# Optimization experiments

Hardware: AMD Instinct MI355X
Metric: run time of the kernel (lower is better)

Reference implementation:

```python
import jax, jax.numpy as jnp
import numpy as np

D_MODEL = 1024
STATE = 16
EXPAND = 2
D_INNER = D_MODEL * EXPAND
KCONV = 4


def setup_inputs() -> dict:
    key = jax.random.key(0)
    ks = jax.random.split(key, 8)
    s = 0.02  # small init scale for stability
    return {
        "x": jax.random.normal(ks[0], (2, 2048, D_MODEL), jnp.float32),
        "W_in": jax.random.normal(ks[1], (2 * D_INNER, D_MODEL), jnp.float32) * s,
        "conv_w": jax.random.normal(ks[2], (D_INNER, 1, KCONV), jnp.float32) * s,
        "conv_b": jnp.zeros((D_INNER,), jnp.float32),
        # A negative so exp(delta*A) <= 1 (stable recurrence, as in real Mamba init)
        "A": -jnp.abs(jax.random.normal(ks[3], (D_INNER, STATE), jnp.float32)),
        "W_x": jax.random.normal(ks[4], (2 * STATE + 1, D_INNER), jnp.float32) * s,
        "W_dt": jax.random.normal(ks[5], (D_INNER, 1), jnp.float32) * s,
        "b_dt": jnp.zeros((D_INNER,), jnp.float32),
        "W_out": jax.random.normal(ks[6], (D_MODEL, D_INNER), jnp.float32) * s,
    }


def reference(x, W_in, conv_w, conv_b, A, W_x, W_dt, b_dt, W_out):
    B, L, _ = x.shape
    N = A.shape[1]

    # in_proj, split into x-branch and gate z
    xz = jnp.einsum('bld,ed->ble', x, W_in)            # (B,L,2*d_inner)
    xi, z = jnp.split(xz, 2, axis=-1)

    # causal depthwise conv1d (torch: pad=3, kernel=4, truncate to L == left-pad 3, valid)
    xc = jnp.transpose(xi, (0, 2, 1))                  # (B,d_inner,L)
    xc = jnp.pad(xc, ((0, 0), (0, 0), (KCONV - 1, 0)))
    xc = jax.lax.conv_general_dilated(
        xc, conv_w, window_strides=(1,), padding='VALID',
        dimension_numbers=('NCH', 'OIH', 'NCH'),
        feature_group_count=conv_w.shape[0])
    xc = xc + conv_b[None, :, None]
    u = jax.nn.silu(jnp.transpose(xc, (0, 2, 1)))      # (B,L,d_inner)

    # input-dependent delta, B, C
    x_dbl = jnp.einsum('bld,ed->ble', u, W_x)          # (B,L,2N+1)
    dlt, Bm, Cm = jnp.split(x_dbl, [1, 1 + N], axis=-1)
    delta = jax.nn.softplus(dlt @ W_dt.T + b_dt)       # (B,L,d_inner)

    # selective scan over time
    def step(h, inp):
        u_t, d_t, B_t, C_t = inp                       # (B,d),(B,d),(B,N),(B,N)
        A_bar = jnp.exp(d_t[..., None] * A)            # (B,d,N)
        h = A_bar * h + (d_t * u_t)[..., None] * B_t[:, None, :]
        y = jnp.einsum('bdn,bn->bd', h, C_t)
        return h, y

    h0 = jnp.zeros((B, A.shape[0], N), u.dtype)
    xs = (jnp.swapaxes(u, 0, 1), jnp.swapaxes(delta, 0, 1),
          jnp.swapaxes(Bm, 0, 1), jnp.swapaxes(Cm, 0, 1))
    _, ys = jax.lax.scan(step, h0, xs)                 # ys: (L,B,d_inner)
    y = jnp.swapaxes(ys, 0, 1)

    y = y * jax.nn.silu(z)
    return jnp.einsum('bld,md->blm', y, W_out)
```

## Files before the change

kernel.cpp:

```cpp
#include <hip/hip_runtime.h>
#include <hip/hip_bf16.h>

#define BATCH   2
#define LSEQ    2048
#define DMODEL  1024
#define DINNER  2048
#define NST     16

#define LC      64
#define NCHUNK  (LSEQ / LC)

#define LOG2E   1.4426950408889634f
#define RLOG2E  0.6931471805599453f

typedef __bf16 bf16x8 __attribute__((ext_vector_type(8)));
typedef float  f32x4  __attribute__((ext_vector_type(4)));

__device__ __forceinline__ unsigned short f2bf(float f) {
  unsigned int u = __float_as_uint(f);
  return (unsigned short)((u + 0x7FFFu + ((u >> 16) & 1u)) >> 16);
}

__device__ __forceinline__ float fast_exp2(float x) {
#if __has_builtin(__builtin_amdgcn_exp2f)
  return __builtin_amdgcn_exp2f(x);
#else
  float r; asm("v_exp_f32 %0, %1\ns_nop 0" : "=v"(r) : "v"(x)); return r;
#endif
}
__device__ __forceinline__ float fast_log2(float x) {
#if __has_builtin(__builtin_amdgcn_logf)
  return __builtin_amdgcn_logf(x);
#else
  float r; asm("v_log_f32 %0, %1\ns_nop 0" : "=v"(r) : "v"(x)); return r;
#endif
}
__device__ __forceinline__ float fast_softplus(float x) {
  float ex = fast_exp2(x * LOG2E);
  return fast_log2(1.0f + ex) * RLOG2E;
}

__device__ __forceinline__ void async_copy16(const void* g, void* l) {
  __builtin_amdgcn_global_load_lds((__attribute__((address_space(1))) void*)g,
                                   (__attribute__((address_space(3))) void*)l,
                                   16, 0, 0);
}

__global__ __launch_bounds__(256) void cvt_bf16(const float4* __restrict__ in,
                                                ushort4* __restrict__ o, int n4) {
  int i = blockIdx.x * 256 + threadIdx.x;
  if (i >= n4) return;
  float4 v = in[i];
  ushort4 r;
  r.x = f2bf(v.x); r.y = f2bf(v.y); r.z = f2bf(v.z); r.w = f2bf(v.w);
  o[i] = r;
}

template<int N, int BN, int K>
__global__ __launch_bounds__(256, 2) void gemm_bf16(const unsigned short* __restrict__ A,
                                                    const unsigned short* __restrict__ B,
                                                    float* __restrict__ C) {
  constexpr int NB = BN / 32;
  __shared__ unsigned short As[128][64];
  __shared__ unsigned short Bs[BN][64];
  const int tid  = threadIdx.x;
  const int wave = tid >> 6;
  const int lane = tid & 63;
  const int row0 = blockIdx.y * 128;
  const int col0 = blockIdx.x * BN;
  const int wr   = (wave >> 1) * 64;
  const int wc   = (wave & 1)  * (BN / 2);
  const int fr   = lane & 15;
  const int fq   = lane >> 4;

  f32x4 acc[4][NB] = {};

  const int sr = wave * 8 + (lane >> 3);
  const int gp = lane & 7;
  const int sgl = gp ^ (sr & 7);
  const unsigned short* gA = A + (size_t)(row0 + sr) * K + sgl * 8;
  const unsigned short* gB = B + (size_t)(col0 + sr) * K + sgl * 8;
  char* lA = (char*)As + wave * 1024;
  char* lB = (char*)Bs + wave * 1024;

  const int rsw = (fr & 7);

  for (int k0 = 0; k0 < K; k0 += 64) {
    #pragma unroll
    for (int c = 0; c < 4; ++c)
      async_copy16(gA + (size_t)c * 32 * K + k0, lA + c * 4096);
    #pragma unroll
    for (int c = 0; c < NB; ++c)
      async_copy16(gB + (size_t)c * 32 * K + k0, lB + c * 4096);
    __syncthreads();

    #pragma unroll
    for (int kk = 0; kk < 2; ++kk) {
      bf16x8 af[4], bfr[NB];
      #pragma unroll
      for (int i = 0; i < 4; ++i)
        af[i] = *(const bf16x8*)((const char*)As + (wr + i * 16 + fr) * 128 +
                                 (((kk << 2) | fq) ^ rsw) * 16);
      #pragma unroll
      for (int j = 0; j < NB; ++j)
        bfr[j] = *(const bf16x8*)((const char*)Bs + (wc + j * 16 + fr) * 128 +
                                  (((kk << 2) | fq) ^ rsw) * 16);
      #pragma unroll
      for (int i = 0; i < 4; ++i)
        #pragma unroll
        for (int j = 0; j < NB; ++j)
          acc[i][j] = __builtin_amdgcn_mfma_f32_16x16x32_bf16(af[i], bfr[j], acc[i][j], 0, 0, 0);
    }
    __syncthreads();
  }

  #pragma unroll
  for (int i = 0; i < 4; ++i)
    #pragma unroll
    for (int j = 0; j < NB; ++j) {
      int row = row0 + wr + i * 16 + fq * 4;
      int col = col0 + wc + j * 16 + fr;
      #pragma unroll
      for (int r = 0; r < 4; ++r)
        C[(size_t)(row + r) * N + col] = acc[i][j][r];
    }
}

__global__ __launch_bounds__(256) void conv_kernel(const float* __restrict__ xz,
                                                   const float* __restrict__ cw,
                                                   const float* __restrict__ cb,
                                                   float* __restrict__ u) {
  size_t i = (size_t)blockIdx.x * 256 + threadIdx.x;
  int d4 = (int)(i & (DINNER / 4 - 1));
  int t2 = (int)((i >> 9) & (LSEQ / 2 - 1));
  int b  = (int)(i >> 19);
  int d  = d4 * 4;
  int t0 = t2 * 2;

  float4 w0 = *(const float4*)(cw + (d + 0) * 4);
  float4 w1 = *(const float4*)(cw + (d + 1) * 4);
  float4 w2 = *(const float4*)(cw + (d + 2) * 4);
  float4 w3 = *(const float4*)(cw + (d + 3) * 4);
  float4 bias = *(const float4*)(cb + d);

  size_t base = ((size_t)b * LSEQ + t0) * (2 * DINNER) + d;
  const float4 zero = make_float4(0.f, 0.f, 0.f, 0.f);
  float4 xm3 = (t0 >= 3) ? *(const float4*)(xz + base - 3 * (2 * DINNER)) : zero;
  float4 xm2 = (t0 >= 2) ? *(const float4*)(xz + base - 2 * (2 * DINNER)) : zero;
  float4 xm1 = (t0 >= 1) ? *(const float4*)(xz + base - 1 * (2 * DINNER)) : zero;
  float4 x00 = *(const float4*)(xz + base);
  float4 xp1 = *(const float4*)(xz + base + (2 * DINNER));

  float4 s0, s1;
  s0.x = bias.x + w0.x * xm3.x + w0.y * xm2.x + w0.z * xm1.x + w0.w * x00.x;
  s0.y = bias.y + w1.x * xm3.y + w1.y * xm2.y + w1.z * xm1.y + w1.w * x00.y;
  s0.z = bias.z + w2.x * xm3.z + w2.y * xm2.z + w2.z * xm1.z + w2.w * x00.z;
  s0.w = bias.w + w3.x * xm3.w + w3.y * xm2.w + w3.z * xm1.w + w3.w * x00.w;
  s1.x = bias.x + w0.x * xm2.x + w0.y * xm1.x + w0.z * x00.x + w0.w * xp1.x;
  s1.y = bias.y + w1.x * xm2.y + w1.y * xm1.y + w1.z * x00.y + w1.w * xp1.y;
  s1.z = bias.z + w2.x * xm2.z + w2.y * xm1.z + w2.z * x00.z + w2.w * xp1.z;
  s1.w = bias.w + w3.x * xm2.w + w3.y * xm1.w + w3.z * x00.w + w3.w * xp1.w;

  float4 r0, r1;
  r0.x = s0.x / (1.0f + __expf(-s0.x));
  r0.y = s0.y / (1.0f + __expf(-s0.y));
  r0.z = s0.z / (1.0f + __expf(-s0.z));
  r0.w = s0.w / (1.0f + __expf(-s0.w));
  r1.x = s1.x / (1.0f + __expf(-s1.x));
  r1.y = s1.y / (1.0f + __expf(-s1.y));
  r1.z = s1.z / (1.0f + __expf(-s1.z));
  r1.w = s1.w / (1.0f + __expf(-s1.w));

  size_t uo = ((size_t)b * LSEQ + t0) * DINNER + d;
  *(float4*)(u + uo)          = r0;
  *(float4*)(u + uo + DINNER) = r1;
}

__global__ __launch_bounds__(256, 2) void xdbl_kernel(const float* __restrict__ u,
                                                      const float* __restrict__ Wx,
                                                      float* __restrict__ xz,
                                                      float* __restrict__ bc) {
  const int tid  = threadIdx.x;
  const int wave = tid >> 6;
  const int lane = tid & 63;
  const int row0 = blockIdx.x * 4;

  float acc[9][4];
  #pragma unroll
  for (int i = 0; i < 9; ++i)
    #pragma unroll
    for (int r = 0; r < 4; ++r) acc[i][r] = 0.0f;

  const float* up    = u  + (size_t)row0 * DINNER + lane * 4;
  const float* wbase = Wx + (size_t)wave * 8 * DINNER + lane * 4;
  const float* w32   = Wx + (size_t)32 * DINNER + lane * 4;

  for (int kt = 0; kt < 8; ++kt) {
    const int ko = kt * 256;
    float4 uv0 = *(const float4*)(up + 0 * DINNER + ko);
    float4 uv1 = *(const float4*)(up + 1 * DINNER + ko);
    float4 uv2 = *(const float4*)(up + 2 * DINNER + ko);
    float4 uv3 = *(const float4*)(up + 3 * DINNER + ko);
    #pragma unroll
    for (int i = 0; i < 9; ++i) {
      float4 w = (i < 8) ? *(const float4*)(wbase + (size_t)i * DINNER + ko)
                         : *(const float4*)(w32 + ko);
      acc[i][0] = fmaf(uv0.x, w.x, fmaf(uv0.y, w.y, fmaf(uv0.z, w.z, fmaf(uv0.w, w.w, acc[i][0]))));
      acc[i][1] = fmaf(uv1.x, w.x, fmaf(uv1.y, w.y, fmaf(uv1.z, w.z, fmaf(uv1.w, w.w, acc[i][1]))));
      acc[i][2] = fmaf(uv2.x, w.x, fmaf(uv2.y, w.y, fmaf(uv2.z, w.z, fmaf(uv2.w, w.w, acc[i][2]))));
      acc[i][3] = fmaf(uv3.x, w.x, fmaf(uv3.y, w.y, fmaf(uv3.z, w.z, fmaf(uv3.w, w.w, acc[i][3]))));
    }
  }

  #pragma unroll
  for (int i = 0; i < 9; ++i)
    #pragma unroll
    for (int r = 0; r < 4; ++r)
      #pragma unroll
      for (int m = 1; m < 64; m <<= 1)
        acc[i][r] += __shfl_xor(acc[i][r], m);

  #pragma unroll
  for (int r = 0; r < 4; ++r) {
    if (lane == r) {
      const size_t row = row0 + r;
      #pragma unroll
      for (int i = 0; i < 8; ++i) {
        const int e = wave * 8 + i;
        if (e == 0) xz[row * (2 * DINNER)] = acc[i][r];
        else        bc[row * 32 + (e - 1)] = acc[i][r];
      }
      if (wave == 0) bc[row * 32 + 31] = acc[8][r];
    }
  }
}

__global__ __launch_bounds__(256) void scanA(const float* __restrict__ u,
                                             const float* __restrict__ xz,
                                             const float* __restrict__ bc,
                                             const float* __restrict__ Amat,
                                             const float* __restrict__ Wdt,
                                             const float* __restrict__ bdt,
                                             float* __restrict__ Pbuf,
                                             float* __restrict__ Wbuf) {
  __shared__ float sB[LC][16];
  __shared__ float sdlt[LC];
  const int tid  = threadIdx.x;
  const int dblk = blockIdx.x & 7;
  const int c    = (blockIdx.x >> 3) & (NCHUNK - 1);
  const int b    = blockIdx.x >> 8;
  const int d    = dblk * 256 + tid;
  const int t0   = c * LC;

  {
    int r = tid >> 2, cp = (tid & 3) * 4;
    *(float4*)&sB[r][cp] = *(const float4*)(bc + ((size_t)(b * LSEQ + t0) + r) * 32 + cp);
    if (tid < LC) sdlt[tid] = xz[(size_t)(b * LSEQ + t0 + tid) * (2 * DINNER)];
  }

  const float wd = Wdt[d];
  const float bd = bdt[d];
  float A2[16];
  #pragma unroll
  for (int i = 0; i < 4; ++i) {
    float4 v = *(const float4*)(Amat + (size_t)d * 16 + i * 4);
    A2[i*4+0] = v.x * LOG2E; A2[i*4+1] = v.y * LOG2E;
    A2[i*4+2] = v.z * LOG2E; A2[i*4+3] = v.w * LOG2E;
  }
  float h[16];
  #pragma unroll
  for (int n = 0; n < 16; ++n) h[n] = 0.0f;
  float S = 0.0f;

  size_t gu = ((size_t)b * LSEQ + t0) * DINNER + d;
  float u0 = u[gu], u1 = u[gu + DINNER];
  __syncthreads();

  auto body = [&](float uc, int ttl) {
    float dl = fast_softplus(fmaf(sdlt[ttl], wd, bd));
    float Bv[16];
    *(float4*)&Bv[0]  = *(const float4*)&sB[ttl][0];
    *(float4*)&Bv[4]  = *(const float4*)&sB[ttl][4];
    *(float4*)&Bv[8]  = *(const float4*)&sB[ttl][8];
    *(float4*)&Bv[12] = *(const float4*)&sB[ttl][12];
    S += dl;
    float dlu = dl * uc;
    #pragma unroll
    for (int n = 0; n < 16; ++n) {
      float ab = fast_exp2(dl * A2[n]);
      h[n] = fmaf(ab, h[n], dlu * Bv[n]);
    }
  };

  for (int tt = 0; tt < LC; tt += 2) {
    float u2 = u[gu + 2 * DINNER], u3 = u[gu + 3 * DINNER];
    body(u0, tt);
    body(u1, tt + 1);
    u0 = u2; u1 = u3;
    gu += 2 * DINNER;
  }

  size_t o = ((size_t)(b * DINNER + d) * NCHUNK + c) * 16;
  float P[16];
  #pragma unroll
  for (int n = 0; n < 16; ++n) P[n] = fast_exp2(A2[n] * S);
  #pragma unroll
  for (int i = 0; i < 4; ++i) {
    *(float4*)(Pbuf + o + i * 4) = make_float4(P[i*4], P[i*4+1], P[i*4+2], P[i*4+3]);
    *(float4*)(Wbuf + o + i * 4) = make_float4(h[i*4], h[i*4+1], h[i*4+2], h[i*4+3]);
  }
}

__global__ __launch_bounds__(256) void scanB(float* __restrict__ Pbuf,
                                             const float* __restrict__ Wbuf) {
  const int lane_id = blockIdx.x * 256 + threadIdx.x;
  const int gc = lane_id >> 4;
  const int n  = lane_id & 15;
  const size_t base = (size_t)gc * NCHUNK * 16 + n;
  float P[NCHUNK], W[NCHUNK];
  #pragma unroll
  for (int c = 0; c < NCHUNK; ++c) {
    P[c] = Pbuf[base + (size_t)c * 16];
    W[c] = Wbuf[base + (size_t)c * 16];
  }
  float h = 0.0f;
  #pragma unroll
  for (int c = 0; c < NCHUNK; ++c) {
    float hin = h;
    h = P[c] * h + W[c];
    Pbuf[base + (size_t)c * 16] = hin;
  }
}

__global__ __launch_bounds__(256) void scanC(float* __restrict__ u,
                                             const float* __restrict__ xz,
                                             const float* __restrict__ bc,
                                             const float* __restrict__ Amat,
                                             const float* __restrict__ Wdt,
                                             const float* __restrict__ bdt,
                                             const float* __restrict__ Hin) {
  __shared__ float sbc[LC][32];
  __shared__ float sdlt[LC];
  const int tid  = threadIdx.x;
  const int dblk = blockIdx.x & 7;
  const int c    = (blockIdx.x >> 3) & (NCHUNK - 1);
  const int b    = blockIdx.x >> 8;
  const int d    = dblk * 256 + tid;
  const int t0   = c * LC;

  {
    const float4* src = (const float4*)(bc + ((size_t)b * LSEQ + t0) * 32);
    ((float4*)sbc)[tid]       = src[tid];
    ((float4*)sbc)[tid + 256] = src[tid + 256];
    if (tid < LC) sdlt[tid] = xz[(size_t)(b * LSEQ + t0 + tid) * (2 * DINNER)];
  }

  const float wd = Wdt[d];
  const float bd = bdt[d];
  float A2[16];
  #pragma unroll
  for (int i = 0; i < 4; ++i) {
    float4 v = *(const float4*)(Amat + (size_t)d * 16 + i * 4);
    A2[i*4+0] = v.x * LOG2E; A2[i*4+1] = v.y * LOG2E;
    A2[i*4+2] = v.z * LOG2E; A2[i*4+3] = v.w * LOG2E;
  }
  const size_t o = ((size_t)(b * DINNER + d) * NCHUNK + c) * 16;
  float h[16];
  #pragma unroll
  for (int i = 0; i < 4; ++i) {
    float4 v = *(const float4*)(Hin + o + i * 4);
    h[i*4+0] = v.x; h[i*4+1] = v.y; h[i*4+2] = v.z; h[i*4+3] = v.w;
  }

  size_t gu = ((size_t)b * LSEQ + t0) * DINNER + d;
  size_t gx = ((size_t)b * LSEQ + t0) * (2 * DINNER) + DINNER + d;

  float u0 = u[gu],  u1 = u[gu + DINNER];
  float z0 = xz[gx], z1 = xz[gx + 2 * DINNER];
  __syncthreads();

  auto body = [&](float uc, float zc, int ttl, size_t cu) {
    float dl = fast_softplus(fmaf(sdlt[ttl], wd, bd));
    float Bv[16], Cv[16];
    *(float4*)&Bv[0]  = *(const float4*)&sbc[ttl][0];
    *(float4*)&Bv[4]  = *(const float4*)&sbc[ttl][4];
    *(float4*)&Bv[8]  = *(const float4*)&sbc[ttl][8];
    *(float4*)&Bv[12] = *(const float4*)&sbc[ttl][12];
    *(float4*)&Cv[0]  = *(const float4*)&sbc[ttl][16];
    *(float4*)&Cv[4]  = *(const float4*)&sbc[ttl][20];
    *(float4*)&Cv[8]  = *(const float4*)&sbc[ttl][24];
    *(float4*)&Cv[12] = *(const float4*)&sbc[ttl][28];
    float dlu = dl * uc;
    float y = 0.0f;
    #pragma unroll
    for (int n = 0; n < 16; ++n) {
      float ab = fast_exp2(dl * A2[n]);
      h[n] = fmaf(ab, h[n], dlu * Bv[n]);
      y = fmaf(h[n], Cv[n], y);
    }
    float sig = 1.0f / (1.0f + __expf(-zc));
    u[cu] = y * zc * sig;
  };

  for (int tt = 0; tt < LC; tt += 2) {
    float u2 = u[gu + 2 * DINNER],  u3 = u[gu + 3 * DINNER];
    float z2 = xz[gx + 4 * DINNER], z3 = xz[gx + 6 * DINNER];
    body(u0, z0, tt,     gu);
    body(u1, z1, tt + 1, gu + DINNER);
    u0 = u2; u1 = u3; z0 = z2; z1 = z3;
    gu += 2 * DINNER; gx += 4 * DINNER;
  }
}

extern "C" void kernel_launch(void* const* d_in, const int* in_sizes, int n_in,
                              void* d_out, int out_size, void* d_ws, size_t ws_size,
                              hipStream_t stream) {
  const float* x      = (const float*)d_in[0];
  const float* W_in   = (const float*)d_in[1];
  const float* conv_w = (const float*)d_in[2];
  const float* conv_b = (const float*)d_in[3];
  const float* A      = (const float*)d_in[4];
  const float* W_x    = (const float*)d_in[5];
  const float* W_dt   = (const float*)d_in[6];
  const float* b_dt   = (const float*)d_in[7];
  const float* W_out  = (const float*)d_in[8];
  float* out = (float*)d_out;

  float* ws = (float*)d_ws;
  float* xz = ws;
  float* u  = xz + (size_t)BATCH * LSEQ * 2 * DINNER;
  float* bc = u  + (size_t)BATCH * LSEQ * DINNER;
  float* Pb = bc + (size_t)BATCH * LSEQ * 32;
  float* Wb = Pb + (size_t)BATCH * DINNER * NCHUNK * 16;

  const int ML = BATCH * LSEQ;

  unsigned short* x_bf    = (unsigned short*)Pb;
  unsigned short* win_bf  = (unsigned short*)Wb;
  unsigned short* y_bf    = (unsigned short*)Pb;
  unsigned short* wout_bf = (unsigned short*)xz;

  cvt_bf16<<<(ML * DMODEL / 4) / 256, 256, 0, stream>>>((const float4*)x,    (ushort4*)x_bf,   ML * DMODEL / 4);
  cvt_bf16<<<(2 * DINNER * DMODEL / 4) / 256, 256, 0, stream>>>((const float4*)W_in, (ushort4*)win_bf, 2 * DINNER * DMODEL / 4);
  gemm_bf16<2 * DINNER, 128, DMODEL><<<dim3((2 * DINNER) / 128, ML / 128), 256, 0, stream>>>(x_bf, win_bf, xz);
  conv_kernel<<<(ML * DINNER / 8) / 256, 256, 0, stream>>>(xz, conv_w, conv_b, u);
  xdbl_kernel<<<ML / 4, 256, 0, stream>>>(u, W_x, xz, bc);
  scanA<<<BATCH * NCHUNK * 8, 256, 0, stream>>>(u, xz, bc, A, W_dt, b_dt, Pb, Wb);
  scanB<<<(BATCH * DINNER * NST) / 256, 256, 0, stream>>>(Pb, Wb);
  scanC<<<BATCH * NCHUNK * 8, 256, 0, stream>>>(u, xz, bc, A, W_dt, b_dt, Pb);
  cvt_bf16<<<(ML * DINNER / 4) / 256, 256, 0, stream>>>((const float4*)u,     (ushort4*)y_bf,    ML * DINNER / 4);
  cvt_bf16<<<(DMODEL * DINNER / 4) / 256, 256, 0, stream>>>((const float4*)W_out, (ushort4*)wout_bf, DMODEL * DINNER / 4);
  gemm_bf16<DMODEL, 64, DINNER><<<dim3(DMODEL / 64, ML / 128), 256, 0, stream>>>(y_bf, wout_bf, out);
}
```

Before: 211.6 us.

## Halve scan chunk length, store chunk delta sums, swizzle GEMM tile order

The scan chunk length drops from 64 to 32, doubling the number of chunk blocks to give more parallelism in scanA and scanC. scanA now writes only the per-chunk delta sum instead of the 16 decay factors, and scanB recomputes the decays with exp2 while updating Wbuf in place. This cuts carry-buffer traffic but makes the serial cross-chunk pass twice as long. The GEMMs also remap block IDs into a grouped order, aiming for better L2 reuse, and the workspace aliases are rearranged to fit the new buffer sizes.

```diff
diff --git a/kernel.cpp b/kernel.cpp
--- a/kernel.cpp
+++ b/kernel.cpp
@@ -7,7 +7,7 @@
 #define DINNER  2048
 #define NST     16
 
-#define LC      64
+#define LC      32
 #define NCHUNK  (LSEQ / LC)
 
 #define LOG2E   1.4426950408889634f
@@ -60,14 +60,18 @@
 __global__ __launch_bounds__(256, 2) void gemm_bf16(const unsigned short* __restrict__ A,
                                                     const unsigned short* __restrict__ B,
                                                     float* __restrict__ C) {
-  constexpr int NB = BN / 32;
+  constexpr int NB  = BN / 32;
+  constexpr int GX  = N / BN;
+  constexpr int NWG = GX * 32;
   __shared__ unsigned short As[128][64];
   __shared__ unsigned short Bs[BN][64];
   const int tid  = threadIdx.x;
   const int wave = tid >> 6;
   const int lane = tid & 63;
-  const int row0 = blockIdx.y * 128;
-  const int col0 = blockIdx.x * BN;
+  const int bid  = blockIdx.y * GX + blockIdx.x;
+  const int swz  = (bid & 7) * (NWG / 8) + (bid >> 3);
+  const int row0 = (swz / GX) * 128;
+  const int col0 = (swz % GX) * BN;
   const int wr   = (wave >> 1) * 64;
   const int wc   = (wave & 1)  * (BN / 2);
   const int fr   = lane & 15;
@@ -75,8 +79,8 @@
 
   f32x4 acc[4][NB] = {};
 
-  const int sr = wave * 8 + (lane >> 3);
-  const int gp = lane & 7;
+  const int sr  = wave * 8 + (lane >> 3);
+  const int gp  = lane & 7;
   const int sgl = gp ^ (sr & 7);
   const unsigned short* gA = A + (size_t)(row0 + sr) * K + sgl * 8;
   const unsigned short* gB = B + (size_t)(col0 + sr) * K + sgl * 8;
@@ -241,22 +245,22 @@
                                              const float* __restrict__ Amat,
                                              const float* __restrict__ Wdt,
                                              const float* __restrict__ bdt,
-                                             float* __restrict__ Pbuf,
+                                             float* __restrict__ Sbuf,
                                              float* __restrict__ Wbuf) {
   __shared__ float sB[LC][16];
   __shared__ float sdlt[LC];
   const int tid  = threadIdx.x;
   const int dblk = blockIdx.x & 7;
   const int c    = (blockIdx.x >> 3) & (NCHUNK - 1);
-  const int b    = blockIdx.x >> 8;
+  const int b    = blockIdx.x >> 9;
   const int d    = dblk * 256 + tid;
   const int t0   = c * LC;
 
-  {
+  if (tid < LC * 4) {
     int r = tid >> 2, cp = (tid & 3) * 4;
     *(float4*)&sB[r][cp] = *(const float4*)(bc + ((size_t)(b * LSEQ + t0) + r) * 32 + cp);
-    if (tid < LC) sdlt[tid] = xz[(size_t)(b * LSEQ + t0 + tid) * (2 * DINNER)];
-  }
+  }
+  if (tid < LC) sdlt[tid] = xz[(size_t)(b * LSEQ + t0 + tid) * (2 * DINNER)];
 
   const float wd = Wdt[d];
   const float bd = bdt[d];
@@ -300,35 +304,31 @@
     gu += 2 * DINNER;
   }
 
-  size_t o = ((size_t)(b * DINNER + d) * NCHUNK + c) * 16;
-  float P[16];
-  #pragma unroll
-  for (int n = 0; n < 16; ++n) P[n] = fast_exp2(A2[n] * S);
-  #pragma unroll
-  for (int i = 0; i < 4; ++i) {
-    *(float4*)(Pbuf + o + i * 4) = make_float4(P[i*4], P[i*4+1], P[i*4+2], P[i*4+3]);
+  const size_t gc = (size_t)(b * DINNER + d);
+  Sbuf[gc * NCHUNK + c] = S;
+  size_t o = (gc * NCHUNK + c) * 16;
+  #pragma unroll
+  for (int i = 0; i < 4; ++i)
     *(float4*)(Wbuf + o + i * 4) = make_float4(h[i*4], h[i*4+1], h[i*4+2], h[i*4+3]);
-  }
-}
-
-__global__ __launch_bounds__(256) void scanB(float* __restrict__ Pbuf,
-                                             const float* __restrict__ Wbuf) {
+}
+
+__global__ __launch_bounds__(256) void scanB(const float* __restrict__ Sbuf,
+                                             float* __restrict__ Wbuf,
+                                             const float* __restrict__ Amat) {
   const int lane_id = blockIdx.x * 256 + threadIdx.x;
   const int gc = lane_id >> 4;
   const int n  = lane_id & 15;
-  const size_t base = (size_t)gc * NCHUNK * 16 + n;
-  float P[NCHUNK], W[NCHUNK];
-  #pragma unroll
+  const int d  = gc & (DINNER - 1);
+  const float A2 = Amat[(size_t)d * 16 + n] * LOG2E;
+  const float* sp = Sbuf + (size_t)gc * NCHUNK;
+  const size_t wbase = (size_t)gc * NCHUNK * 16 + n;
+  float h = 0.0f;
+  #pragma unroll 8
   for (int c = 0; c < NCHUNK; ++c) {
-    P[c] = Pbuf[base + (size_t)c * 16];
-    W[c] = Wbuf[base + (size_t)c * 16];
-  }
-  float h = 0.0f;
-  #pragma unroll
-  for (int c = 0; c < NCHUNK; ++c) {
+    float P = fast_exp2(A2 * sp[c]);
     float hin = h;
-    h = P[c] * h + W[c];
-    Pbuf[base + (size_t)c * 16] = hin;
+    h = fmaf(P, h, Wbuf[wbase + (size_t)c * 16]);
+    Wbuf[wbase + (size_t)c * 16] = hin;
   }
 }
 
@@ -344,16 +344,12 @@
   const int tid  = threadIdx.x;
   const int dblk = blockIdx.x & 7;
   const int c    = (blockIdx.x >> 3) & (NCHUNK - 1);
-  const int b    = blockIdx.x >> 8;
+  const int b    = blockIdx.x >> 9;
   const int d    = dblk * 256 + tid;
   const int t0   = c * LC;
 
-  {
-    const float4* src = (const float4*)(bc + ((size_t)b * LSEQ + t0) * 32);
-    ((float4*)sbc)[tid]       = src[tid];
-    ((float4*)sbc)[tid + 256] = src[tid + 256];
-    if (tid < LC) sdlt[tid] = xz[(size_t)(b * LSEQ + t0 + tid) * (2 * DINNER)];
-  }
+  ((float4*)sbc)[tid] = ((const float4*)(bc + ((size_t)b * LSEQ + t0) * 32))[tid];
+  if (tid < LC) sdlt[tid] = xz[(size_t)(b * LSEQ + t0 + tid) * (2 * DINNER)];
 
   const float wd = Wdt[d];
   const float bd = bdt[d];
@@ -430,24 +426,24 @@
   float* xz = ws;
   float* u  = xz + (size_t)BATCH * LSEQ * 2 * DINNER;
   float* bc = u  + (size_t)BATCH * LSEQ * DINNER;
-  float* Pb = bc + (size_t)BATCH * LSEQ * 32;
-  float* Wb = Pb + (size_t)BATCH * DINNER * NCHUNK * 16;
+  float* Sb = bc + (size_t)BATCH * LSEQ * 32;
+  float* Wb = Sb + (size_t)BATCH * DINNER * NCHUNK;
 
   const int ML = BATCH * LSEQ;
 
-  unsigned short* x_bf    = (unsigned short*)Pb;
-  unsigned short* win_bf  = (unsigned short*)Wb;
-  unsigned short* y_bf    = (unsigned short*)Pb;
-  unsigned short* wout_bf = (unsigned short*)xz;
+  unsigned short* x_bf    = (unsigned short*)Wb;
+  unsigned short* win_bf  = (unsigned short*)Wb + (size_t)ML * DMODEL;
+  unsigned short* y_bf    = (unsigned short*)xz;
+  unsigned short* wout_bf = (unsigned short*)(xz + (size_t)8 * 1024 * 1024);
 
   cvt_bf16<<<(ML * DMODEL / 4) / 256, 256, 0, stream>>>((const float4*)x,    (ushort4*)x_bf,   ML * DMODEL / 4);
   cvt_bf16<<<(2 * DINNER * DMODEL / 4) / 256, 256, 0, stream>>>((const float4*)W_in, (ushort4*)win_bf, 2 * DINNER * DMODEL / 4);
   gemm_bf16<2 * DINNER, 128, DMODEL><<<dim3((2 * DINNER) / 128, ML / 128), 256, 0, stream>>>(x_bf, win_bf, xz);
   conv_kernel<<<(ML * DINNER / 8) / 256, 256, 0, stream>>>(xz, conv_w, conv_b, u);
   xdbl_kernel<<<ML / 4, 256, 0, stream>>>(u, W_x, xz, bc);
-  scanA<<<BATCH * NCHUNK * 8, 256, 0, stream>>>(u, xz, bc, A, W_dt, b_dt, Pb, Wb);
-  scanB<<<(BATCH * DINNER * NST) / 256, 256, 0, stream>>>(Pb, Wb);
-  scanC<<<BATCH * NCHUNK * 8, 256, 0, stream>>>(u, xz, bc, A, W_dt, b_dt, Pb);
+  scanA<<<BATCH * NCHUNK * 8, 256, 0, stream>>>(u, xz, bc, A, W_dt, b_dt, Sb, Wb);
+  scanB<<<(BATCH * DINNER * NST) / 256, 256, 0, stream>>>(Sb, Wb, A);
+  scanC<<<BATCH * NCHUNK * 8, 256, 0, stream>>>(u, xz, bc, A, W_dt, b_dt, Wb);
   cvt_bf16<<<(ML * DINNER / 4) / 256, 256, 0, stream>>>((const float4*)u,     (ushort4*)y_bf,    ML * DINNER / 4);
   cvt_bf16<<<(DMODEL * DINNER / 4) / 256, 256, 0, stream>>>((const float4*)W_out, (ushort4*)wout_bf, DMODEL * DINNER / 4);
   gemm_bf16<DMODEL, 64, DINNER><<<dim3(DMODEL / 64, ML / 128), 256, 0, stream>>>(y_bf, wout_bf, out);
```

Result: no change. 208.7 us (-1.4%).
